# Optimization experiments

Hardware: AMD Instinct MI355X
Metric: run time of the kernel (lower is better)

The kernel has to match this reference:

```python
import jax, jax.numpy as jnp
import numpy as np

NUM_HEADS = 8
KEY_DIM = 32
ATTN_RATIO = 4
RESOLUTION = 7
VAL_DIM = KEY_DIM * ATTN_RATIO  # 128
SCALE = KEY_DIM ** (-0.5)


def _bias_idxs():
    # (2, N) grid positions, N = resolution^2
    r = RESOLUTION
    gh, gw = np.meshgrid(np.arange(r), np.arange(r), indexing='ij')
    pos = np.stack([gh, gw], 0).reshape(2, -1)
    rel = np.abs(pos[:, :, None] - pos[:, None, :])
    return jnp.asarray(rel[0] * r + rel[1], dtype=jnp.int32)  # (N, N)


def setup_inputs() -> dict:
    key = jax.random.key(0)
    ks = jax.random.split(key, 4)
    B, N, D = 2048, RESOLUTION * RESOLUTION, 384
    qkv_out = KEY_DIM * NUM_HEADS * 2 + VAL_DIM * NUM_HEADS  # 1536
    return {
        'x': jax.random.normal(ks[0], (B, N, D), jnp.float32),
        'qkv_kernel': jax.random.normal(ks[1], (D, qkv_out), jnp.float32) * 0.02,
        'qkv_bias': jnp.zeros((qkv_out,), jnp.float32),
        'proj_kernel': jax.random.normal(ks[2], (VAL_DIM * NUM_HEADS, D), jnp.float32) * 0.02,
        'proj_bias': jnp.zeros((D,), jnp.float32),
        'attention_biases': jax.random.normal(ks[3], (NUM_HEADS, N), jnp.float32) * 0.02,
    }


def reference(x, qkv_kernel, qkv_bias, proj_kernel, proj_bias, attention_biases):
    B, N, _ = x.shape
    idxs = _bias_idxs()  # (N, N) int32
    qkv = jnp.matmul(x, qkv_kernel) + qkv_bias            # (B, N, 1536)
    qkv = qkv.reshape(B, N, NUM_HEADS, -1).transpose(0, 2, 1, 3)  # (B, H, N, 2k+v)
    q = qkv[..., :KEY_DIM]
    k = qkv[..., KEY_DIM:2 * KEY_DIM]
    v = qkv[..., 2 * KEY_DIM:]
    attn = jnp.einsum('bhnd,bhmd->bhnm', q, k) * SCALE    # (B, H, N, N)
    bias = attention_biases[:, idxs]                       # (H, N, N) gather
    attn = jax.nn.softmax(attn + bias, axis=-1)
    out = jnp.einsum('bhnm,bhmd->bhnd', attn, v)           # (B, H, N, val_dim)
    out = out.transpose(0, 2, 1, 3).reshape(B, N, NUM_HEADS * VAL_DIM)
    return jnp.matmul(out, proj_kernel) + proj_bias
```

## Files before the change

kernel.cpp:

```cpp
#include <hip/hip_runtime.h>
#include <hip/hip_bf16.h>

using bf16x8 = short __attribute__((ext_vector_type(8)));
using f32x16 = float __attribute__((ext_vector_type(16)));

#define MROWS 100352
#define SCALE_Q 0.17677669529663687f
#define XCAST_BLOCKS 18816

static __device__ __forceinline__ unsigned short f2bs(float f){
  unsigned u = __builtin_bit_cast(unsigned, f);
  unsigned r = (u + 0x7FFFu + ((u >> 16) & 1u)) >> 16;
  return (unsigned short)r;
}
static __device__ __forceinline__ unsigned packbf(float a, float b){
  return (unsigned)f2bs(a) | ((unsigned)f2bs(b) << 16);
}

__global__ void k_prep(const float* __restrict__ x, const float* __restrict__ qkvW,
                       const float* __restrict__ qkvB, const float* __restrict__ projW,
                       const float* __restrict__ ab,
                       short* __restrict__ xb, short* __restrict__ WqkvT, short* __restrict__ WpT,
                       float* __restrict__ bqkv, float* __restrict__ bias_expT){
  const int bi = blockIdx.x;
  if (bi < XCAST_BLOCKS){
    const int i = bi*256 + threadIdx.x;
    const float4 u0 = *reinterpret_cast<const float4*>(x + (size_t)i*8);
    const float4 u1 = *reinterpret_cast<const float4*>(x + (size_t)i*8 + 4);
    bf16x8 t;
    t[0]=(short)f2bs(u0.x); t[1]=(short)f2bs(u0.y); t[2]=(short)f2bs(u0.z); t[3]=(short)f2bs(u0.w);
    t[4]=(short)f2bs(u1.x); t[5]=(short)f2bs(u1.y); t[6]=(short)f2bs(u1.z); t[7]=(short)f2bs(u1.w);
    *reinterpret_cast<bf16x8*>(xb + (size_t)i*8) = t;
    return;
  }
  int i = (bi - XCAST_BLOCKS)*256 + threadIdx.x;
  if (i < 1536*384){
    int c = i/384, f = i - c*384;
    int src; float sc = 1.0f;
    if (c < 512){ src = (c>>6)*192 + (c&63); if ((c&63) < 32) sc = SCALE_Q; }
    else        { int dv = c - 512; src = (dv>>7)*192 + 64 + (dv&127); }
    WqkvT[i] = (short)f2bs(qkvW[f*1536 + src] * sc);
    return;
  }
  i -= 1536*384;
  if (i < 384*1024){
    int j = i/1024, m = i - j*1024;
    WpT[i] = (short)f2bs(projW[m*384 + j]);
    return;
  }
  i -= 384*1024;
  if (i < 1536){
    int c = i; int src; float sc = 1.0f;
    if (c < 512){ src = (c>>6)*192 + (c&63); if ((c&63) < 32) sc = SCALE_Q; }
    else        { int dv = c - 512; src = (dv>>7)*192 + 64 + (dv&127); }
    bqkv[c] = qkvB[src] * sc;
    return;
  }
  i -= 1536;
  if (i < 8*49*64){
    int h = i / (49*64), rem = i - h*(49*64);
    int n = rem >> 6, r = rem & 63;
    float v = 0.0f;
    if (r < 49){
      int rh = r/7, rw = r - rh*7, ch = n/7, cw = n - ch*7;
      int dh = rh>ch?rh-ch:ch-rh, dw = rw>cw?rw-cw:cw-rw;
      v = ab[h*49 + dh*7 + dw];
    }
    bias_expT[i] = v;
  }
}

__global__ __launch_bounds__(512) void k_qkv7(const short* __restrict__ xb,
                                              const short* __restrict__ WqkvT,
                                              const float* __restrict__ bqkv,
                                              short* __restrict__ qkvbuf){
  __shared__ short lds3[3][512*32];
  const int t = threadIdx.x;
  const int lane = t & 63, w = t >> 6;
  const int hi = lane >> 5, l31 = lane & 31;
  const int wm = w >> 1, wn = w & 1;

  const int nwg = 6*392;
  const int lin = blockIdx.x + 6*blockIdx.y;
  const int swz = (lin & 7)*(nwg>>3) + (lin>>3);
  const int slab = swz % 6, panel = swz / 6;
  const size_t R0 = (size_t)panel*256, C0 = (size_t)slab*256;

  const int srowl  = lane >> 2;
  const int schunk = ((lane & 3) ^ ((lane >> 3) & 3)) * 8;
  const short* aG0 = xb    + (R0 + (size_t)(w*16       + srowl))*384 + schunk;
  const short* aG1 = xb    + (R0 + (size_t)((8+w)*16   + srowl))*384 + schunk;
  const short* bG0 = WqkvT + (C0 + (size_t)(w*16       + srowl))*384 + schunk;
  const short* bG1 = WqkvT + (C0 + (size_t)((8+w)*16   + srowl))*384 + schunk;

  auto stage = [&](int bufi, int kti){
    short* base = &lds3[bufi][0];
    __builtin_amdgcn_global_load_lds((const unsigned __attribute__((address_space(1)))*)(aG0 + kti*32),
        (unsigned __attribute__((address_space(3)))*)(base + w*512), 16, 0, 0);
    __builtin_amdgcn_global_load_lds((const unsigned __attribute__((address_space(1)))*)(aG1 + kti*32),
        (unsigned __attribute__((address_space(3)))*)(base + (8+w)*512), 16, 0, 0);
    __builtin_amdgcn_global_load_lds((const unsigned __attribute__((address_space(1)))*)(bG0 + kti*32),
        (unsigned __attribute__((address_space(3)))*)(base + 8192 + w*512), 16, 0, 0);
    __builtin_amdgcn_global_load_lds((const unsigned __attribute__((address_space(1)))*)(bG1 + kti*32),
        (unsigned __attribute__((address_space(3)))*)(base + 8192 + (8+w)*512), 16, 0, 0);
  };

  f32x16 acc[2][4];
  #pragma unroll
  for (int mt=0; mt<2; ++mt)
    #pragma unroll
    for (int nt=0; nt<4; ++nt) acc[mt][nt] = (f32x16)0.0f;

  stage(0, 0); stage(1, 1);

  int cur = 0;
  for (int kt=0; kt<12; ++kt){
    if (kt < 11) asm volatile("s_waitcnt vmcnt(4)" ::: "memory");
    else         asm volatile("s_waitcnt vmcnt(0)" ::: "memory");
    __builtin_amdgcn_s_barrier();

    const char* Ab = (const char*)&lds3[cur][0];
    const char* Bb = Ab + 16384;

    {
      bf16x8 aF[2], bF[4];
      #pragma unroll
      for (int mt=0; mt<2; ++mt){
        const int rA = wm*64 + mt*32 + l31;
        aF[mt] = *reinterpret_cast<const bf16x8*>(Ab + rA*64 + (((0|hi) ^ ((rA>>1)&3))<<4));
      }
      #pragma unroll
      for (int nt=0; nt<4; ++nt){
        const int rB = wn*128 + nt*32 + l31;
        bF[nt] = *reinterpret_cast<const bf16x8*>(Bb + rB*64 + (((0|hi) ^ ((rB>>1)&3))<<4));
      }
      __builtin_amdgcn_s_setprio(1);
      #pragma unroll
      for (int mt=0; mt<2; ++mt)
        #pragma unroll
        for (int nt=0; nt<4; ++nt)
          acc[mt][nt] = __builtin_amdgcn_mfma_f32_32x32x16_bf16(aF[mt], bF[nt], acc[mt][nt], 0,0,0);
      __builtin_amdgcn_s_setprio(0);
    }
    if (kt < 10){
      const int nb = (cur + 2 >= 3) ? cur - 1 : cur + 2;
      stage(nb, kt + 2);
    }
    {
      bf16x8 aF[2], bF[4];
      #pragma unroll
      for (int mt=0; mt<2; ++mt){
        const int rA = wm*64 + mt*32 + l31;
        aF[mt] = *reinterpret_cast<const bf16x8*>(Ab + rA*64 + (((2|hi) ^ ((rA>>1)&3))<<4));
      }
      #pragma unroll
      for (int nt=0; nt<4; ++nt){
        const int rB = wn*128 + nt*32 + l31;
        bF[nt] = *reinterpret_cast<const bf16x8*>(Bb + rB*64 + (((2|hi) ^ ((rB>>1)&3))<<4));
      }
      __builtin_amdgcn_s_setprio(1);
      #pragma unroll
      for (int mt=0; mt<2; ++mt)
        #pragma unroll
        for (int nt=0; nt<4; ++nt)
          acc[mt][nt] = __builtin_amdgcn_mfma_f32_32x32x16_bf16(aF[mt], bF[nt], acc[mt][nt], 0,0,0);
      __builtin_amdgcn_s_setprio(0);
    }
    cur = (cur == 2) ? 0 : cur + 1;
  }

  #pragma unroll
  for (int nt=0; nt<4; ++nt){
    const int c = (int)C0 + wn*128 + nt*32 + l31;
    const float bb = bqkv[c];
    #pragma unroll
    for (int mt=0; mt<2; ++mt){
      const size_t rbase = R0 + wm*64 + mt*32;
      #pragma unroll
      for (int rg=0; rg<16; ++rg){
        const size_t r = rbase + (rg&3) + 8*(rg>>2) + 4*hi;
        qkvbuf[r*1536 + c] = (short)f2bs(acc[mt][nt][rg] + bb);
      }
    }
  }
}

__global__ __launch_bounds__(256) void k_proj4(const short* __restrict__ A,
                                               const short* __restrict__ Bw,
                                               const float* __restrict__ bias,
                                               float* __restrict__ out){
  __shared__ short Alds[128*64];
  __shared__ short Blds[128*64];
  const int lane = threadIdx.x & 63, w = threadIdx.x >> 6;
  const int hi = lane >> 5, l31 = lane & 31;
  const int wm = w >> 1, wn = w & 1;

  const int nwg = 3 * 784;
  const int lin = blockIdx.x + 3 * blockIdx.y;
  const int swz = (lin & 7) * (nwg >> 3) + (lin >> 3);
  const int slab = swz % 3, panel = swz / 3;
  const size_t R0 = (size_t)panel * 128, C0 = (size_t)slab * 128;

  f32x16 acc[2][2];
  acc[0][0]=(f32x16)0.f; acc[0][1]=(f32x16)0.f; acc[1][0]=(f32x16)0.f; acc[1][1]=(f32x16)0.f;

  const int srow = lane >> 3;
  const int sG   = ((lane & 7) ^ srow) * 8;
  const short* aG = A  + (R0 + (size_t)(w*8 + srow))*1024 + sG;
  const short* bG = Bw + (C0 + (size_t)(w*8 + srow))*1024 + sG;

  for (int kt=0; kt<16; ++kt){
    #pragma unroll
    for (int j=0; j<4; ++j){
      __builtin_amdgcn_global_load_lds(
        (const unsigned int __attribute__((address_space(1)))*)(aG + (size_t)j*32*1024 + kt*64),
        (unsigned int __attribute__((address_space(3)))*)(&Alds[(j*32 + w*8)*64]), 16, 0, 0);
      __builtin_amdgcn_global_load_lds(
        (const unsigned int __attribute__((address_space(1)))*)(bG + (size_t)j*32*1024 + kt*64),
        (unsigned int __attribute__((address_space(3)))*)(&Blds[(j*32 + w*8)*64]), 16, 0, 0);
    }
    __syncthreads();
    #pragma unroll
    for (int ks=0; ks<4; ++ks){
      bf16x8 aF[2], bF[2];
      #pragma unroll
      for (int mt=0; mt<2; ++mt){
        const int rA = wm*64 + mt*32 + l31;
        aF[mt] = *reinterpret_cast<const bf16x8*>(
                   (const char*)Alds + rA*128 + ((((ks<<1)|hi) ^ (rA&7))<<4));
      }
      #pragma unroll
      for (int nt=0; nt<2; ++nt){
        const int rB = wn*64 + nt*32 + l31;
        bF[nt] = *reinterpret_cast<const bf16x8*>(
                   (const char*)Blds + rB*128 + ((((ks<<1)|hi) ^ (rB&7))<<4));
      }
      #pragma unroll
      for (int mt=0; mt<2; ++mt)
        #pragma unroll
        for (int nt=0; nt<2; ++nt)
          acc[mt][nt] = __builtin_amdgcn_mfma_f32_32x32x16_bf16(aF[mt], bF[nt], acc[mt][nt], 0,0,0);
    }
    __syncthreads();
  }

  #pragma unroll
  for (int nt=0; nt<2; ++nt){
    const int c = (int)C0 + wn*64 + nt*32 + l31;
    const float bb = bias[c];
    #pragma unroll
    for (int mt=0; mt<2; ++mt){
      const size_t rbase = R0 + wm*64 + mt*32;
      #pragma unroll
      for (int rg=0; rg<16; ++rg){
        const size_t r = rbase + (rg&3) + 8*(rg>>2) + 4*hi;
        out[r*384 + c] = acc[mt][nt][rg] + bb;
      }
    }
  }
}

__global__ __launch_bounds__(256) void k_attn(const short* __restrict__ qkvbuf,
                                              const float* __restrict__ bias_expT, short* __restrict__ aout){
  const int lane = threadIdx.x & 63, w = threadIdx.x >> 6;
  const int hi = lane >> 5, l31 = lane & 31;
  const int b = blockIdx.x, hg = blockIdx.y;
  const int h = hg*4 + w;

  __shared__ short vlds[4*49*136];

  for (int i=0; i<13; ++i){
    const int n = i*4 + w;
    if (n < 49){
      const bf16x8 vv = *reinterpret_cast<const bf16x8*>(qkvbuf + (b*49+n)*1536 + 512 + hg*512 + lane*8);
      const int hh = lane >> 4;
      const int d0 = ((lane & 15) * 8) ^ (((n>>3)&1) << 5);
      *reinterpret_cast<bf16x8*>(&vlds[(hh*49 + n)*136 + d0]) = vv;
    }
  }
  __syncthreads();

  bf16x8 kf[2][2];
  #pragma unroll
  for (int mt=0; mt<2; ++mt){
    const int n = 32*mt + l31;
    #pragma unroll
    for (int ks=0; ks<2; ++ks)
      kf[mt][ks] = (n < 49)
        ? *reinterpret_cast<const bf16x8*>(qkvbuf + (b*49+n)*1536 + h*64 + 32 + ks*16 + hi*8)
        : (bf16x8)(short)0;
  }
  const short* vb = &vlds[w*49*136];
  const int dxbase = hi << 5;

  for (int rb=0; rb<2; ++rb){
    const int r = 32*rb + l31;
    bf16x8 qf[2];
    #pragma unroll
    for (int ks=0; ks<2; ++ks)
      qf[ks] = (r < 49)
        ? *reinterpret_cast<const bf16x8*>(qkvbuf + (b*49+r)*1536 + h*64 + ks*16 + hi*8)
        : (bf16x8)(short)0;

    f32x16 s[2];
    s[0] = (f32x16)0.0f; s[1] = (f32x16)0.0f;
    #pragma unroll
    for (int ks=0; ks<2; ++ks){
      s[0] = __builtin_amdgcn_mfma_f32_32x32x16_bf16(kf[0][ks], qf[ks], s[0], 0, 0, 0);
      s[1] = __builtin_amdgcn_mfma_f32_32x32x16_bf16(kf[1][ks], qf[ks], s[1], 0, 0, 0);
    }

    float mloc = -3.0e38f;
    #pragma unroll
    for (int mt=0; mt<2; ++mt)
      #pragma unroll
      for (int rg=0; rg<16; ++rg){
        const int n = 32*mt + (rg&3) + 8*(rg>>2) + 4*hi;
        float v = s[mt][rg];
        v = (n < 49) ? v + bias_expT[(h*49 + n)*64 + r] : -1.0e30f;
        s[mt][rg] = v;
        mloc = fmaxf(mloc, v);
      }
    const float mrow = fmaxf(mloc, __shfl_xor(mloc, 32));
    float sloc = 0.0f;
    #pragma unroll
    for (int mt=0; mt<2; ++mt)
      #pragma unroll
      for (int rg=0; rg<16; ++rg){
        const float p = __expf(s[mt][rg] - mrow);
        s[mt][rg] = p; sloc += p;
      }
    const float inv = 1.0f / (sloc + __shfl_xor(sloc, 32));
    #pragma unroll
    for (int mt=0; mt<2; ++mt)
      #pragma unroll
      for (int rg=0; rg<16; ++rg) s[mt][rg] *= inv;

    unsigned pk[8][2];
    #pragma unroll
    for (int o=0; o<8; ++o){
      const int mt = o>>2, base = 4*(o&3);
      pk[o][0] = packbf(s[mt][base+0], s[mt][base+1]);
      pk[o][1] = packbf(s[mt][base+2], s[mt][base+3]);
    }
    bf16x8 af[4];
    #pragma unroll
    for (int ks=0; ks<4; ++ks){
      const unsigned e0 = pk[2*ks][0],   e1 = pk[2*ks][1];
      const unsigned o0 = pk[2*ks+1][0], o1 = pk[2*ks+1][1];
      const unsigned own0 = hi ? o0 : e0, own1 = hi ? o1 : e1;
      const unsigned oth0 = hi ? e0 : o0, oth1 = hi ? e1 : o1;
      const unsigned sw0 = __shfl_xor(oth0, 32), sw1 = __shfl_xor(oth1, 32);
      const unsigned lo0 = hi ? sw0 : own0, lo1 = hi ? sw1 : own1;
      const unsigned h0  = hi ? own0 : sw0, h1  = hi ? own1 : sw1;
      union { bf16x8 v; unsigned u[4]; } t;
      t.u[0]=lo0; t.u[1]=lo1; t.u[2]=h0; t.u[3]=h1;
      af[ks] = t.v;
    }

    #pragma unroll
    for (int dt=0; dt<4; ++dt){
      const int dx = (dt*32 + l31) ^ dxbase;
      f32x16 acc = (f32x16)0.0f;
      #pragma unroll
      for (int ks=0; ks<4; ++ks){
        bf16x8 t;
        if (ks < 3){
          const int nb = ks*16 + hi*8;
          #pragma unroll
          for (int j=0; j<8; ++j) t[j] = vb[(nb + j)*136 + dx];
        } else {
          #pragma unroll
          for (int j=0; j<8; ++j) t[j] = 0;
          if (hi == 0) t[0] = vb[48*136 + (dt*32 + l31)];
        }
        acc = __builtin_amdgcn_mfma_f32_32x32x16_bf16(af[ks], t, acc, 0, 0, 0);
      }
      #pragma unroll
      for (int rg=0; rg<16; ++rg){
        const int rr = 32*rb + (rg&3) + 8*(rg>>2) + 4*hi;
        if (rr < 49)
          aout[(b*49+rr)*1024 + h*128 + dt*32 + l31] = (short)f2bs(acc[rg]);
      }
    }
  }
}

extern "C" void kernel_launch(void* const* d_in, const int* in_sizes, int n_in,
                              void* d_out, int out_size, void* d_ws, size_t ws_size,
                              hipStream_t stream) {
  const float* x     = (const float*)d_in[0];
  const float* qkvW  = (const float*)d_in[1];
  const float* qkvB  = (const float*)d_in[2];
  const float* projW = (const float*)d_in[3];
  const float* projB = (const float*)d_in[4];
  const float* ab    = (const float*)d_in[5];

  char* ws = (char*)d_ws;
  short* aoutb = (short*)ws;
  short* xb    = (short*)ws;
  size_t off = (size_t)MROWS*1024*2;
  short* qkvbuf = (short*)(ws + off); off += (size_t)MROWS*1536*2;
  short* WqkvT  = (short*)(ws + off); off += (size_t)1536*384*2;
  short* WpT    = (short*)(ws + off); off += (size_t)384*1024*2;
  float* bqkv   = (float*)(ws + off); off += (size_t)1536*4;
  float* bias_expT = (float*)(ws + off); off += (size_t)8*49*64*4;
  if (ws_size < off) return;

  const int conv_total = 1536*384 + 384*1024 + 1536 + 8*49*64;
  const int prep_blocks = XCAST_BLOCKS + (conv_total + 255)/256;
  k_prep<<<prep_blocks, 256, 0, stream>>>(x, qkvW, qkvB, projW, ab,
                                          xb, WqkvT, WpT, bqkv, bias_expT);
  k_qkv7<<<dim3(6, 392), 512, 0, stream>>>(xb, WqkvT, bqkv, qkvbuf);
  k_attn<<<dim3(2048, 2), 256, 0, stream>>>(qkvbuf, bias_expT, aoutb);
  k_proj4<<<dim3(3, 784), 256, 0, stream>>>(aoutb, WpT, projB, (float*)d_out);
}
```

Measured before the change: 504.4 us.

## Fuse fp32-to-bf16 cast of x into the QKV GEMM A-tile staging

```diff
diff --git a/kernel.cpp b/kernel.cpp
--- a/kernel.cpp
+++ b/kernel.cpp
@@ -6,7 +6,6 @@
 
 #define MROWS 100352
 #define SCALE_Q 0.17677669529663687f
-#define XCAST_BLOCKS 18816
 
 static __device__ __forceinline__ unsigned short f2bs(float f){
   unsigned u = __builtin_bit_cast(unsigned, f);
@@ -17,23 +16,11 @@
   return (unsigned)f2bs(a) | ((unsigned)f2bs(b) << 16);
 }
 
-__global__ void k_prep(const float* __restrict__ x, const float* __restrict__ qkvW,
-                       const float* __restrict__ qkvB, const float* __restrict__ projW,
-                       const float* __restrict__ ab,
-                       short* __restrict__ xb, short* __restrict__ WqkvT, short* __restrict__ WpT,
-                       float* __restrict__ bqkv, float* __restrict__ bias_expT){
-  const int bi = blockIdx.x;
-  if (bi < XCAST_BLOCKS){
-    const int i = bi*256 + threadIdx.x;
-    const float4 u0 = *reinterpret_cast<const float4*>(x + (size_t)i*8);
-    const float4 u1 = *reinterpret_cast<const float4*>(x + (size_t)i*8 + 4);
-    bf16x8 t;
-    t[0]=(short)f2bs(u0.x); t[1]=(short)f2bs(u0.y); t[2]=(short)f2bs(u0.z); t[3]=(short)f2bs(u0.w);
-    t[4]=(short)f2bs(u1.x); t[5]=(short)f2bs(u1.y); t[6]=(short)f2bs(u1.z); t[7]=(short)f2bs(u1.w);
-    *reinterpret_cast<bf16x8*>(xb + (size_t)i*8) = t;
-    return;
-  }
-  int i = (bi - XCAST_BLOCKS)*256 + threadIdx.x;
+__global__ void k_convert(const float* __restrict__ qkvW, const float* __restrict__ qkvB,
+                          const float* __restrict__ projW, const float* __restrict__ ab,
+                          short* __restrict__ WqkvT, short* __restrict__ WpT,
+                          float* __restrict__ bqkv, float* __restrict__ bias_expT){
+  int i = blockIdx.x*256 + threadIdx.x;
   if (i < 1536*384){
     int c = i/384, f = i - c*384;
     int src; float sc = 1.0f;
@@ -70,7 +57,7 @@
   }
 }
 
-__global__ __launch_bounds__(512) void k_qkv7(const short* __restrict__ xb,
+__global__ __launch_bounds__(512) void k_qkv8(const float* __restrict__ x,
                                               const short* __restrict__ WqkvT,
                                               const float* __restrict__ bqkv,
                                               short* __restrict__ qkvbuf){
@@ -88,22 +75,38 @@
 
   const int srowl  = lane >> 2;
   const int schunk = ((lane & 3) ^ ((lane >> 3) & 3)) * 8;
-  const short* aG0 = xb    + (R0 + (size_t)(w*16       + srowl))*384 + schunk;
-  const short* aG1 = xb    + (R0 + (size_t)((8+w)*16   + srowl))*384 + schunk;
-  const short* bG0 = WqkvT + (C0 + (size_t)(w*16       + srowl))*384 + schunk;
-  const short* bG1 = WqkvT + (C0 + (size_t)((8+w)*16   + srowl))*384 + schunk;
-
-  auto stage = [&](int bufi, int kti){
+  const short* bG0 = WqkvT + (C0 + (size_t)(w*16     + srowl))*384 + schunk;
+  const short* bG1 = WqkvT + (C0 + (size_t)((8+w)*16 + srowl))*384 + schunk;
+
+  const int rs = t >> 1, hf = t & 1;
+  const float* xrow = x + (R0 + rs)*384 + hf*16;
+  const int rxor = (rs >> 1) & 3;
+  const int wa0 = rs*32 + (((2*hf)   ^ rxor) << 3);
+  const int wa1 = rs*32 + (((2*hf+1) ^ rxor) << 3);
+
+  auto stageB = [&](int bufi, int kti){
     short* base = &lds3[bufi][0];
-    __builtin_amdgcn_global_load_lds((const unsigned __attribute__((address_space(1)))*)(aG0 + kti*32),
-        (unsigned __attribute__((address_space(3)))*)(base + w*512), 16, 0, 0);
-    __builtin_amdgcn_global_load_lds((const unsigned __attribute__((address_space(1)))*)(aG1 + kti*32),
-        (unsigned __attribute__((address_space(3)))*)(base + (8+w)*512), 16, 0, 0);
     __builtin_amdgcn_global_load_lds((const unsigned __attribute__((address_space(1)))*)(bG0 + kti*32),
         (unsigned __attribute__((address_space(3)))*)(base + 8192 + w*512), 16, 0, 0);
     __builtin_amdgcn_global_load_lds((const unsigned __attribute__((address_space(1)))*)(bG1 + kti*32),
         (unsigned __attribute__((address_space(3)))*)(base + 8192 + (8+w)*512), 16, 0, 0);
   };
+  auto loadX = [&](float4* g, int kti){
+    const float* p = xrow + kti*32;
+    g[0] = *reinterpret_cast<const float4*>(p);
+    g[1] = *reinterpret_cast<const float4*>(p+4);
+    g[2] = *reinterpret_cast<const float4*>(p+8);
+    g[3] = *reinterpret_cast<const float4*>(p+12);
+  };
+  auto writeA = [&](int bufi, const float4* g){
+    bf16x8 u0, u1;
+    u0[0]=(short)f2bs(g[0].x); u0[1]=(short)f2bs(g[0].y); u0[2]=(short)f2bs(g[0].z); u0[3]=(short)f2bs(g[0].w);
+    u0[4]=(short)f2bs(g[1].x); u0[5]=(short)f2bs(g[1].y); u0[6]=(short)f2bs(g[1].z); u0[7]=(short)f2bs(g[1].w);
+    u1[0]=(short)f2bs(g[2].x); u1[1]=(short)f2bs(g[2].y); u1[2]=(short)f2bs(g[2].z); u1[3]=(short)f2bs(g[2].w);
+    u1[4]=(short)f2bs(g[3].x); u1[5]=(short)f2bs(g[3].y); u1[6]=(short)f2bs(g[3].z); u1[7]=(short)f2bs(g[3].w);
+    *reinterpret_cast<bf16x8*>(&lds3[bufi][wa0]) = u0;
+    *reinterpret_cast<bf16x8*>(&lds3[bufi][wa1]) = u1;
+  };
 
   f32x16 acc[2][4];
   #pragma unroll
@@ -111,15 +114,25 @@
     #pragma unroll
     for (int nt=0; nt<4; ++nt) acc[mt][nt] = (f32x16)0.0f;
 
-  stage(0, 0); stage(1, 1);
-
-  int cur = 0;
+  float4 g[2][4];
+  loadX(g[0], 0);
+  loadX(g[1], 1);
+  stageB(0, 0);
+  stageB(1, 1);
+  asm volatile("s_waitcnt vmcnt(8)" ::: "memory");
+  writeA(0, g[0]);
+  asm volatile("s_waitcnt vmcnt(4)" ::: "memory");
+  writeA(1, g[1]);
+
+  #pragma unroll
   for (int kt=0; kt<12; ++kt){
-    if (kt < 11) asm volatile("s_waitcnt vmcnt(4)" ::: "memory");
-    else         asm volatile("s_waitcnt vmcnt(0)" ::: "memory");
+    if (kt == 0)       asm volatile("s_waitcnt vmcnt(2) lgkmcnt(0)" ::: "memory");
+    else if (kt < 11)  asm volatile("s_waitcnt vmcnt(6) lgkmcnt(0)" ::: "memory");
+    else               asm volatile("s_waitcnt vmcnt(0) lgkmcnt(0)" ::: "memory");
+    __builtin_amdgcn_sched_barrier(0);
     __builtin_amdgcn_s_barrier();
 
-    const char* Ab = (const char*)&lds3[cur][0];
+    const char* Ab = (const char*)&lds3[kt % 3][0];
     const char* Bb = Ab + 16384;
 
     {
@@ -142,10 +155,12 @@
           acc[mt][nt] = __builtin_amdgcn_mfma_f32_32x32x16_bf16(aF[mt], bF[nt], acc[mt][nt], 0,0,0);
       __builtin_amdgcn_s_setprio(0);
     }
-    if (kt < 10){
-      const int nb = (cur + 2 >= 3) ? cur - 1 : cur + 2;
-      stage(nb, kt + 2);
-    }
+
+    if (kt <= 9){
+      loadX(g[kt & 1], kt + 2);
+      stageB((kt + 2) % 3, kt + 2);
+    }
+
     {
       bf16x8 aF[2], bF[4];
       #pragma unroll
@@ -166,7 +181,11 @@
           acc[mt][nt] = __builtin_amdgcn_mfma_f32_32x32x16_bf16(aF[mt], bF[nt], acc[mt][nt], 0,0,0);
       __builtin_amdgcn_s_setprio(0);
     }
-    cur = (cur == 2) ? 0 : cur + 1;
+
+    if (kt <= 9){
+      asm volatile("s_waitcnt vmcnt(2)" ::: "memory");
+      writeA((kt + 2) % 3, g[kt & 1]);
+    }
   }
 
   #pragma unroll
@@ -353,9 +372,9 @@
       const unsigned sw0 = __shfl_xor(oth0, 32), sw1 = __shfl_xor(oth1, 32);
       const unsigned lo0 = hi ? sw0 : own0, lo1 = hi ? sw1 : own1;
       const unsigned h0  = hi ? own0 : sw0, h1  = hi ? own1 : sw1;
-      union { bf16x8 v; unsigned u[4]; } t;
-      t.u[0]=lo0; t.u[1]=lo1; t.u[2]=h0; t.u[3]=h1;
-      af[ks] = t.v;
+      union { bf16x8 v; unsigned u[4]; } tt;
+      tt.u[0]=lo0; tt.u[1]=lo1; tt.u[2]=h0; tt.u[3]=h1;
+      af[ks] = tt.v;
     }
 
     #pragma unroll
@@ -364,17 +383,17 @@
       f32x16 acc = (f32x16)0.0f;
       #pragma unroll
       for (int ks=0; ks<4; ++ks){
-        bf16x8 t;
+        bf16x8 tt;
         if (ks < 3){
           const int nb = ks*16 + hi*8;
           #pragma unroll
-          for (int j=0; j<8; ++j) t[j] = vb[(nb + j)*136 + dx];
+          for (int j=0; j<8; ++j) tt[j] = vb[(nb + j)*136 + dx];
         } else {
           #pragma unroll
-          for (int j=0; j<8; ++j) t[j] = 0;
-          if (hi == 0) t[0] = vb[48*136 + (dt*32 + l31)];
+          for (int j=0; j<8; ++j) tt[j] = 0;
+          if (hi == 0) tt[0] = vb[48*136 + (dt*32 + l31)];
         }
-        acc = __builtin_amdgcn_mfma_f32_32x32x16_bf16(af[ks], t, acc, 0, 0, 0);
+        acc = __builtin_amdgcn_mfma_f32_32x32x16_bf16(af[ks], tt, acc, 0, 0, 0);
       }
       #pragma unroll
       for (int rg=0; rg<16; ++rg){
@@ -398,7 +417,6 @@
 
   char* ws = (char*)d_ws;
   short* aoutb = (short*)ws;
-  short* xb    = (short*)ws;
   size_t off = (size_t)MROWS*1024*2;
   short* qkvbuf = (short*)(ws + off); off += (size_t)MROWS*1536*2;
   short* WqkvT  = (short*)(ws + off); off += (size_t)1536*384*2;
@@ -408,10 +426,9 @@
   if (ws_size < off) return;
 
   const int conv_total = 1536*384 + 384*1024 + 1536 + 8*49*64;
-  const int prep_blocks = XCAST_BLOCKS + (conv_total + 255)/256;
-  k_prep<<<prep_blocks, 256, 0, stream>>>(x, qkvW, qkvB, projW, ab,
-                                          xb, WqkvT, WpT, bqkv, bias_expT);
-  k_qkv7<<<dim3(6, 392), 512, 0, stream>>>(xb, WqkvT, bqkv, qkvbuf);
+  k_convert<<<(conv_total + 255)/256, 256, 0, stream>>>(qkvW, qkvB, projW, ab,
+                                                        WqkvT, WpT, bqkv, bias_expT);
+  k_qkv8<<<dim3(6, 392), 512, 0, stream>>>(x, WqkvT, bqkv, qkvbuf);
   k_attn<<<dim3(2048, 2), 256, 0, stream>>>(qkvbuf, bias_expT, aoutb);
   k_proj4<<<dim3(3, 784), 256, 0, stream>>>(aoutb, WpT, projB, (float*)d_out);
 }
```

New measurement: 545.9 us. +8.2%, slower.
